# Kernel tuning notes

Measured on AMD Instinct MI355X. Metric: run time of the kernel, lower is better.

Reference implementation:

```python
import jax, jax.numpy as jnp
import numpy as np

B, T, D_IN, UNITS, D_OUT = 64, 2048, 64, 128, 1
ODE_UNFOLDS = 6  # fused semi-implicit Euler sub-steps per timestep


def setup_inputs() -> dict:
    key = jax.random.key(0)
    ks = jax.random.split(key, 8)
    s = lambda fan: 1.0 / np.sqrt(fan).astype(np.float32)
    return {
        "x": jax.random.normal(ks[0], (B, T, D_IN), jnp.float32),
        "kernel": jax.random.normal(ks[1], (D_IN, UNITS), jnp.float32) * s(D_IN),
        "recurrent_kernel": jax.random.normal(ks[2], (UNITS, UNITS), jnp.float32) * s(UNITS),
        "bias": jnp.zeros((UNITS,), jnp.float32),
        "tau": jax.random.uniform(ks[3], (UNITS,), jnp.float32, 0.5, 2.0),  # positive time constants
        "A": jax.random.normal(ks[4], (UNITS,), jnp.float32),  # reversal potentials
        "out_kernel": jax.random.normal(ks[5], (UNITS, D_OUT), jnp.float32) * s(UNITS),
        "out_bias": jnp.zeros((D_OUT,), jnp.float32),
    }


def _ltc_scan(x_proj, recurrent_kernel, tau, A):
    # x_proj: [B, T, U] precomputed input projection (+bias)
    dt = jnp.float32(1.0 / ODE_UNFOLDS)
    inv_tau = 1.0 / tau  # [U]

    def step(h, xp):  # h: [B,U], xp: [B,U]
        # LTC fused ODE solver: semi-implicit Euler, ODE_UNFOLDS sub-steps
        for _ in range(ODE_UNFOLDS):
            f = jax.nn.sigmoid(xp + h @ recurrent_kernel)  # gating nonlinearity
            h = (h + dt * f * A) / (1.0 + dt * (inv_tau + f))
        return h, h

    h0 = jnp.zeros((x_proj.shape[0], tau.shape[0]), x_proj.dtype)
    _, hs = jax.lax.scan(step, h0, jnp.swapaxes(x_proj, 0, 1))  # scan over time
    return jnp.swapaxes(hs, 0, 1)  # [B, T, U]


def reference(x, kernel, recurrent_kernel, bias, tau, A, out_kernel, out_bias):
    # input projection hoisted out of the recurrence (invariant across unfolds)
    x_proj = jnp.einsum("bti,iu->btu", x, kernel) + bias  # [B,T,U]
    hs = _ltc_scan(x_proj, recurrent_kernel, tau, A)       # return_sequences=True
    return hs @ out_kernel + out_bias                       # Dense(output_dim) -> [B,T,1]
```

## Files before the change

### kernel.cpp

```cpp
#include <hip/hip_runtime.h>

#define TSTEPS  2048
#define DIN     64
#define UNITS   128
#define UNFOLDS 6
#define NT      512
#define CSTR    20


template <int CTRL>
__device__ __forceinline__ float dpp_f(float v) {
    return __int_as_float(
        __builtin_amdgcn_mov_dpp(__float_as_int(v), CTRL, 0xF, 0xF, true));
}

__global__ __launch_bounds__(NT) void ltc_kernel(
    const float* __restrict__ x,
    const float* __restrict__ kern,
    const float* __restrict__ rk,
    const float* __restrict__ bias,
    const float* __restrict__ tau,
    const float* __restrict__ Avec,
    const float* __restrict__ okern,
    const float* __restrict__ obias,
    float* __restrict__ out)
{
    const int b    = blockIdx.x;
    const int tid  = threadIdx.x;
    const int p    = tid & 15;
    const int g    = tid >> 4;
    const int wid  = tid >> 6;
    const int lane = tid & 63;

    __shared__ __align__(16) float hbuf[2][16 * CSTR];
    __shared__ float part[8];

    float w_[8][4];
    #pragma unroll
    for (int m = 0; m < 8; ++m) {
        float4 v = ((const float4*)(rk + (size_t)(8 * p + m) * UNITS))[g];
        w_[m][0] = v.x; w_[m][1] = v.y; w_[m][2] = v.z; w_[m][3] = v.w;
    }
    float kk_[4][4];
    #pragma unroll
    for (int m = 0; m < 4; ++m) {
        float4 v = ((const float4*)(kern + (size_t)(4 * p + m) * UNITS))[g];
        kk_[m][0] = v.x; kk_[m][1] = v.y; kk_[m][2] = v.z; kk_[m][3] = v.w;
    }

    const float dt  = 1.0f / 6.0f;
    const int   sel = ((p & 1) << 1) | ((p >> 1) & 1);
    const int   u_own = 4 * g + sel;
    const float dtA_o  = dt * Avec[u_own];
    const float cden_o = 1.0f + dt / tau[u_own];
    const float cdp_o  = cden_o + dt;
    const float ok_o   = okern[u_own];
    float4 bv = ((const float4*)bias)[g];
    float bias4[4] = {bv.x, bv.y, bv.z, bv.w};
    const float ob = obias[0];

    const int waddr = CSTR * (u_own >> 3) + (u_own & 7);

    float h_own = 0.0f;
    if (tid < 16 * CSTR) hbuf[0][tid] = 0.0f;

    const float* xb = x + (size_t)b * TSTEPS * DIN;
    float4 xr = *(const float4*)(xb + 4 * p);
    __syncthreads();

    for (int t = 0; t < TSTEPS; ++t) {
        float xp[4];
        #pragma unroll
        for (int i = 0; i < 4; ++i) xp[i] = (p == 0) ? bias4[i] : 0.0f;
        {
            float xrf[4] = {xr.x, xr.y, xr.z, xr.w};
            #pragma unroll
            for (int m = 0; m < 4; ++m)
                #pragma unroll
                for (int i = 0; i < 4; ++i)
                    xp[i] = fmaf(xrf[m], kk_[m][i], xp[i]);
        }
        int tn = (t + 1 < TSTEPS) ? t + 1 : t;
        float4 xn = *(const float4*)(xb + (size_t)tn * DIN + 4 * p);

        #pragma unroll
        for (int s = 0; s < UNFOLDS; ++s) {
            const float4* hv = (const float4*)&hbuf[s & 1][CSTR * p];
            float4 h0 = hv[0], h1 = hv[1];
            float hf[8] = {h0.x, h0.y, h0.z, h0.w, h1.x, h1.y, h1.z, h1.w};

            float acc[4] = {xp[0], xp[1], xp[2], xp[3]};
            #pragma unroll
            for (int m = 0; m < 8; ++m)
                #pragma unroll
                for (int i = 0; i < 4; ++i)
                    acc[i] = fmaf(hf[m], w_[m][i], acc[i]);

            const bool b0 = (p & 1) != 0;
            const bool b1 = (p & 2) != 0;
            float a0 = b0 ? acc[2] : acc[0];
            float c0 = b0 ? acc[0] : acc[2];
            float r0 = a0 + dpp_f<0xB1>(c0);
            float a1 = b0 ? acc[3] : acc[1];
            float c1 = b0 ? acc[1] : acc[3];
            float r1 = a1 + dpp_f<0xB1>(c1);
            float a2 = b1 ? r1 : r0;
            float c2 = b1 ? r0 : r1;
            float sv = a2 + dpp_f<0x4E>(c2);
            sv += dpp_f<0x124>(sv);
            sv += dpp_f<0x128>(sv);

            float e   = __expf(-sv);
            float num = fmaf(h_own, e, h_own + dtA_o);
            float den = fmaf(cden_o, e, cdp_o);
            h_own = num * __builtin_amdgcn_rcpf(den);

            if (p < 4) hbuf[(s & 1) ^ 1][waddr] = h_own;

            if (s == UNFOLDS - 1) {
                float q = (p < 4) ? h_own * ok_o : 0.0f;
                q += __shfl_xor(q, 1);
                q += __shfl_xor(q, 2);
                q += __shfl_xor(q, 4);
                q += __shfl_xor(q, 8);
                q += __shfl_xor(q, 16);
                q += __shfl_xor(q, 32);
                if (lane == 0) part[wid] = q;
            }

            asm volatile("s_waitcnt lgkmcnt(0)" ::: "memory");
            __builtin_amdgcn_sched_barrier(0);
            __builtin_amdgcn_s_barrier();
            __builtin_amdgcn_sched_barrier(0);
        }

        if (tid == 0) {
            float r = ob;
            #pragma unroll
            for (int k = 0; k < 8; ++k) r += part[k];
            out[(size_t)b * TSTEPS + t] = r;
        }
        xr = xn;
    }
}

extern "C" void kernel_launch(void* const* d_in, const int* in_sizes, int n_in,
                              void* d_out, int out_size, void* d_ws, size_t ws_size,
                              hipStream_t stream) {
    const float* x     = (const float*)d_in[0];
    const float* kern  = (const float*)d_in[1];
    const float* rk    = (const float*)d_in[2];
    const float* bias  = (const float*)d_in[3];
    const float* tau   = (const float*)d_in[4];
    const float* Avec  = (const float*)d_in[5];
    const float* okern = (const float*)d_in[6];
    const float* obias = (const float*)d_in[7];
    float* out = (float*)d_out;

    ltc_kernel<<<64, NT, 0, stream>>>(
        x, kern, rk, bias, tau, Avec, okern, obias, out);
}
```

Before: 3.818 ms.

## Halve block size so each thread computes eight recurrent units

The kernel now runs 256 threads per block instead of 512. Each thread accumulates 8 output columns and owns two hidden units, so the recurrent matvec, reduction and update are widened accordingly. The shared h buffer and the output reduction are remapped, with part of the output sum moved from shuffles to DPP. The aim is fewer waves taking part in the per-unfold block barrier and less LDS traffic. The cost is twice the FMA work per thread on the serial critical path and higher register pressure.

```diff
diff --git a/kernel.cpp b/kernel.cpp
--- a/kernel.cpp
+++ b/kernel.cpp
@@ -4,8 +4,7 @@
 #define DIN     64
 #define UNITS   128
 #define UNFOLDS 6
-#define NT      512
-#define CSTR    20
+#define NT      256
 
 
 template <int CTRL>
@@ -32,97 +31,114 @@
     const int wid  = tid >> 6;
     const int lane = tid & 63;
 
-    __shared__ __align__(16) float hbuf[2][16 * CSTR];
-    __shared__ float part[8];
+    __shared__ __align__(16) float hbuf[2][192];
+    __shared__ float part[4];
 
-    float w_[8][4];
+    float w_[8][8];
     #pragma unroll
     for (int m = 0; m < 8; ++m) {
-        float4 v = ((const float4*)(rk + (size_t)(8 * p + m) * UNITS))[g];
-        w_[m][0] = v.x; w_[m][1] = v.y; w_[m][2] = v.z; w_[m][3] = v.w;
+        const float* row = rk + (size_t)(8 * p + m) * UNITS + 8 * g;
+        #pragma unroll
+        for (int j = 0; j < 8; ++j) w_[m][j] = row[j];
     }
-    float kk_[4][4];
+    float kk_[4][8];
     #pragma unroll
     for (int m = 0; m < 4; ++m) {
-        float4 v = ((const float4*)(kern + (size_t)(4 * p + m) * UNITS))[g];
-        kk_[m][0] = v.x; kk_[m][1] = v.y; kk_[m][2] = v.z; kk_[m][3] = v.w;
+        const float* row = kern + (size_t)(4 * p + m) * UNITS + 8 * g;
+        #pragma unroll
+        for (int j = 0; j < 8; ++j) kk_[m][j] = row[j];
     }
+    float bias_[8];
+    #pragma unroll
+    for (int j = 0; j < 8; ++j) bias_[j] = (p == 0) ? bias[8 * g + j] : 0.0f;
 
+    const int   u0  = ((p & 1) << 2) | (p & 2);
+    const int   ua  = 8 * g + u0;
     const float dt  = 1.0f / 6.0f;
-    const int   sel = ((p & 1) << 1) | ((p >> 1) & 1);
-    const int   u_own = 4 * g + sel;
-    const float dtA_o  = dt * Avec[u_own];
-    const float cden_o = 1.0f + dt / tau[u_own];
-    const float cdp_o  = cden_o + dt;
-    const float ok_o   = okern[u_own];
-    float4 bv = ((const float4*)bias)[g];
-    float bias4[4] = {bv.x, bv.y, bv.z, bv.w};
-    const float ob = obias[0];
+    float2 Af = *(const float2*)(Avec + ua);
+    float2 Tf = *(const float2*)(tau + ua);
+    float2 Of = *(const float2*)(okern + ua);
+    const float dtA0 = dt * Af.x, dtA1 = dt * Af.y;
+    const float cd0  = 1.0f + dt / Tf.x, cd1 = 1.0f + dt / Tf.y;
+    const float cp0  = cd0 + dt, cp1 = cd1 + dt;
+    const float ok0  = Of.x, ok1 = Of.y;
+    const float ob   = obias[0];
+    const int   waddr = 12 * g + u0;
 
-    const int waddr = CSTR * (u_own >> 3) + (u_own & 7);
-
-    float h_own = 0.0f;
-    if (tid < 16 * CSTR) hbuf[0][tid] = 0.0f;
+    float h0 = 0.0f, h1 = 0.0f;
+    for (int i = tid; i < 192; i += NT) { hbuf[0][i] = 0.0f; hbuf[1][i] = 0.0f; }
 
     const float* xb = x + (size_t)b * TSTEPS * DIN;
     float4 xr = *(const float4*)(xb + 4 * p);
     __syncthreads();
 
     for (int t = 0; t < TSTEPS; ++t) {
-        float xp[4];
+        float xp[8];
         #pragma unroll
-        for (int i = 0; i < 4; ++i) xp[i] = (p == 0) ? bias4[i] : 0.0f;
+        for (int j = 0; j < 8; ++j) xp[j] = bias_[j];
         {
             float xrf[4] = {xr.x, xr.y, xr.z, xr.w};
             #pragma unroll
             for (int m = 0; m < 4; ++m)
                 #pragma unroll
-                for (int i = 0; i < 4; ++i)
-                    xp[i] = fmaf(xrf[m], kk_[m][i], xp[i]);
+                for (int j = 0; j < 8; ++j)
+                    xp[j] = fmaf(xrf[m], kk_[m][j], xp[j]);
         }
         int tn = (t + 1 < TSTEPS) ? t + 1 : t;
         float4 xn = *(const float4*)(xb + (size_t)tn * DIN + 4 * p);
 
         #pragma unroll
         for (int s = 0; s < UNFOLDS; ++s) {
-            const float4* hv = (const float4*)&hbuf[s & 1][CSTR * p];
-            float4 h0 = hv[0], h1 = hv[1];
-            float hf[8] = {h0.x, h0.y, h0.z, h0.w, h1.x, h1.y, h1.z, h1.w};
+            const float4* hv = (const float4*)&hbuf[s & 1][12 * p];
+            float4 ha = hv[0], hc = hv[1];
+            float hf[8] = {ha.x, ha.y, ha.z, ha.w, hc.x, hc.y, hc.z, hc.w};
 
-            float acc[4] = {xp[0], xp[1], xp[2], xp[3]};
+            float acc[8];
+            #pragma unroll
+            for (int j = 0; j < 8; ++j) acc[j] = xp[j];
             #pragma unroll
             for (int m = 0; m < 8; ++m)
                 #pragma unroll
-                for (int i = 0; i < 4; ++i)
-                    acc[i] = fmaf(hf[m], w_[m][i], acc[i]);
+                for (int j = 0; j < 8; ++j)
+                    acc[j] = fmaf(hf[m], w_[m][j], acc[j]);
 
-            const bool b0 = (p & 1) != 0;
-            const bool b1 = (p & 2) != 0;
-            float a0 = b0 ? acc[2] : acc[0];
-            float c0 = b0 ? acc[0] : acc[2];
-            float r0 = a0 + dpp_f<0xB1>(c0);
-            float a1 = b0 ? acc[3] : acc[1];
-            float c1 = b0 ? acc[1] : acc[3];
-            float r1 = a1 + dpp_f<0xB1>(c1);
-            float a2 = b1 ? r1 : r0;
-            float c2 = b1 ? r0 : r1;
-            float sv = a2 + dpp_f<0x4E>(c2);
-            sv += dpp_f<0x124>(sv);
-            sv += dpp_f<0x128>(sv);
+            const bool q0 = (p & 1) != 0;
+            const bool q1 = (p & 2) != 0;
+            float r_[4];
+            #pragma unroll
+            for (int j = 0; j < 4; ++j) {
+                float mine = q0 ? acc[j + 4] : acc[j];
+                float send = q0 ? acc[j] : acc[j + 4];
+                r_[j] = mine + dpp_f<0xB1>(send);
+            }
+            float s0, s1;
+            {
+                float m0 = q1 ? r_[2] : r_[0];
+                float e0 = q1 ? r_[0] : r_[2];
+                s0 = m0 + dpp_f<0x4E>(e0);
+                float m1 = q1 ? r_[3] : r_[1];
+                float e1 = q1 ? r_[1] : r_[3];
+                s1 = m1 + dpp_f<0x4E>(e1);
+            }
+            s0 += dpp_f<0x124>(s0);  s0 += dpp_f<0x128>(s0);
+            s1 += dpp_f<0x124>(s1);  s1 += dpp_f<0x128>(s1);
 
-            float e   = __expf(-sv);
-            float num = fmaf(h_own, e, h_own + dtA_o);
-            float den = fmaf(cden_o, e, cdp_o);
-            h_own = num * __builtin_amdgcn_rcpf(den);
+            float e0v = __expf(-s0);
+            h0 = fmaf(h0, e0v, h0 + dtA0) *
+                 __builtin_amdgcn_rcpf(fmaf(cd0, e0v, cp0));
+            float e1v = __expf(-s1);
+            h1 = fmaf(h1, e1v, h1 + dtA1) *
+                 __builtin_amdgcn_rcpf(fmaf(cd1, e1v, cp1));
 
-            if (p < 4) hbuf[(s & 1) ^ 1][waddr] = h_own;
+            if (p < 4) {
+                float2 st; st.x = h0; st.y = h1;
+                *(float2*)&hbuf[(s & 1) ^ 1][waddr] = st;
+            }
 
             if (s == UNFOLDS - 1) {
-                float q = (p < 4) ? h_own * ok_o : 0.0f;
-                q += __shfl_xor(q, 1);
-                q += __shfl_xor(q, 2);
-                q += __shfl_xor(q, 4);
-                q += __shfl_xor(q, 8);
+                float q = fmaf(h0, ok0, h1 * ok1);
+                q += dpp_f<0xB1>(q);
+                q += dpp_f<0x4E>(q);
                 q += __shfl_xor(q, 16);
                 q += __shfl_xor(q, 32);
                 if (lane == 0) part[wid] = q;
@@ -134,12 +150,8 @@
             __builtin_amdgcn_sched_barrier(0);
         }
 
-        if (tid == 0) {
-            float r = ob;
-            #pragma unroll
-            for (int k = 0; k < 8; ++k) r += part[k];
-            out[(size_t)b * TSTEPS + t] = r;
-        }
+        if (tid == 0)
+            out[(size_t)b * TSTEPS + t] = part[0] + part[1] + part[2] + part[3] + ob;
         xr = xn;
     }
 }
```

Result: slower. 4.235 ms (+10.9%).
